# Kernel tuning notes

Measured on AMD Instinct MI355X. Metric: run time of the kernel, lower is better.

## Reference

```python
import jax, jax.numpy as jnp
import numpy as np

N, K, D = 65536, 1024, 512


def setup_inputs() -> dict:
    key = jax.random.key(0)
    kx, kc, kv, kp = jax.random.split(key, 4)
    X = jax.random.normal(kx, (N, D), dtype=jnp.float32)
    center = jax.random.normal(kc, (K, D), dtype=jnp.float32)
    var = jax.random.uniform(kv, (K,), dtype=jnp.float32)
    pr = jax.random.uniform(kp, (K,), dtype=jnp.float32)
    threshold = jnp.zeros((1,), dtype=jnp.float32)
    return {"X": X, "center": center, "var": var, "pr": pr, "threshold": threshold}


def reference(X, center, var, pr, threshold):
    # Pairwise squared distances [N, K] via the expanded form
    # avoids materializing the N x K x D tensor).
    x_sq = jnp.sum(X * X, axis=-1, keepdims=True)            # [N, 1]
    c_sq = jnp.sum(center * center, axis=-1)                  # [K]
    cross = jnp.einsum('nd,kd->nk', X, center)                # [N, K]
    sqdist = x_sq - 2.0 * cross + c_sq[None, :]               # [N, K]
    # density: reciprocal-distance weighted sum with weights pr * var
    density = jnp.reciprocal(sqdist) @ (pr * var)             # [N]
    return density - threshold                                 # [N] (threshold [1] broadcasts)
```

## Files before the change

### kernel.cpp

```cpp
#include <hip/hip_runtime.h>
#include <stdint.h>


#define NR 65536
#define KC 1024
#define DD 512

#define BM 128
#define BN 256
#define BK 32
#define NKT (DD / BK)
#define NPART (KC / BN)

#define SLOT_SZ 24576
#define PART_OFF 49152
#define LDS_TOTAL (PART_OFF + 2048)

typedef __bf16 bf16;
typedef __attribute__((ext_vector_type(4))) __bf16 bf16x4;
typedef __attribute__((ext_vector_type(8))) __bf16 bf16x8;
typedef __attribute__((ext_vector_type(4))) float f32x4;

__device__ __forceinline__ void gload16(const void* g, void* l) {
  __builtin_amdgcn_global_load_lds(
      (const __attribute__((address_space(1))) unsigned int*)g,
      (__attribute__((address_space(3))) unsigned int*)l, 16, 0, 0);
}

__global__ __launch_bounds__(256) void prep_kernel(
    const float* __restrict__ X, const float* __restrict__ C,
    const float* __restrict__ var, const float* __restrict__ pr,
    bf16* __restrict__ Xb, bf16* __restrict__ Cb,
    float* __restrict__ xsq, float* __restrict__ csq, float* __restrict__ w) {
  const int row  = (int)((blockIdx.x * 256 + threadIdx.x) >> 6);
  const int lane = (int)(threadIdx.x & 63);
  const bool isX = row < NR;
  const float* srow = isX ? (X + (size_t)row * DD) : (C + (size_t)(row - NR) * DD);
  bf16* drow = isX ? (Xb + (size_t)row * DD) : (Cb + (size_t)(row - NR) * DD);

  float4 a = reinterpret_cast<const float4*>(srow)[lane];
  float4 b = reinterpret_cast<const float4*>(srow)[64 + lane];
  float s = a.x * a.x + a.y * a.y + a.z * a.z + a.w * a.w +
            b.x * b.x + b.y * b.y + b.z * b.z + b.w * b.w;
#pragma unroll
  for (int off = 1; off < 64; off <<= 1) s += __shfl_xor(s, off, 64);

  bf16x4 va = {(bf16)a.x, (bf16)a.y, (bf16)a.z, (bf16)a.w};
  bf16x4 vb = {(bf16)b.x, (bf16)b.y, (bf16)b.z, (bf16)b.w};
  reinterpret_cast<bf16x4*>(drow)[lane]      = va;
  reinterpret_cast<bf16x4*>(drow)[64 + lane] = vb;

  if (lane == 0) {
    if (isX) {
      xsq[row] = s;
    } else {
      const int k = row - NR;
      csq[k] = s;
      w[k]   = pr[k] * var[k];
    }
  }
}


#define STAGE(tn, slotW)                                                        \
  gload16(aSrc0 + (tn) * 32,                smem + (slotW) + wid * 1024);       \
  gload16(aSrc0 + (size_t)64 * DD + (tn) * 32,                                  \
          smem + (slotW) + 4096 + wid * 1024);                                  \
  gload16(bSrc0 + (tn) * 32,                smem + (slotW) + 8192 + wid * 1024);\
  gload16(bSrc0 + (size_t)64 * DD + (tn) * 32,                                  \
          smem + (slotW) + 12288 + wid * 1024);                                 \
  gload16(bSrc0 + (size_t)128 * DD + (tn) * 32,                                 \
          smem + (slotW) + 16384 + wid * 1024);                                 \
  gload16(bSrc0 + (size_t)192 * DD + (tn) * 32,                                 \
          smem + (slotW) + 20480 + wid * 1024);

__global__ __launch_bounds__(256, 2) void density_kernel(
    const bf16* __restrict__ Xb, const bf16* __restrict__ Cb,
    const float* __restrict__ xsq, const float* __restrict__ csq,
    const float* __restrict__ w, float* __restrict__ partial) {
  extern __shared__ char smem[];

  const int tid  = (int)threadIdx.x;
  const int lane = tid & 63;
  const int wid  = tid >> 6;
  const int lr   = lane & 15;
  const int lc   = lane >> 4;

  const int bid   = (int)blockIdx.x;
  const int swz   = (bid & 7) * 256 + (bid >> 3);
  const int ntile = swz >> 9;
  const int mtile = swz & 511;
  const int rowBase = mtile * BM;
  const int colBase = ntile * BN;

  const int chunkSw = (((lane & 3) ^ ((lane >> 3) & 3)) << 3);
  const bf16* aSrc0 = Xb + (size_t)(rowBase + wid * 16 + (lane >> 2)) * DD + chunkSw;
  const bf16* bSrc0 = Cb + (size_t)(colBase + wid * 16 + (lane >> 2)) * DD + chunkSw;

  const int rdSw = ((lc ^ ((lr >> 1) & 3)) << 4);
  const int aRd  = lr * 64 + rdSw;
  const int bRd  = 8192 + (wid * 64 + lr) * 64 + rdSw;

  f32x4 acc[8][4];
#pragma unroll
  for (int m = 0; m < 8; ++m)
#pragma unroll
    for (int n = 0; n < 4; ++n) acc[m][n] = (f32x4){0.f, 0.f, 0.f, 0.f};

  STAGE(0, 0);
  asm volatile("s_waitcnt vmcnt(0)");
  __builtin_amdgcn_s_barrier();

#pragma unroll 1
  for (int t = 0; t < NKT; ++t) {
    const int slotR = (t & 1) ? SLOT_SZ : 0;
    const int slotW = slotR ^ SLOT_SZ;
    const int tn = t + 1;
    const bool st = tn < NKT;

    if (st) {
      STAGE(tn, slotW);
    }

    bf16x8 bg[4];
#pragma unroll
    for (int n = 0; n < 4; ++n)
      bg[n] = *(const bf16x8*)(smem + slotR + bRd + n * 1024);

    __builtin_amdgcn_s_setprio(1);
#pragma unroll
    for (int mi = 0; mi < 8; ++mi) {
      const bf16x8 a = *(const bf16x8*)(smem + slotR + aRd + mi * 1024);
#pragma unroll
      for (int n = 0; n < 4; ++n)
        acc[mi][n] = __builtin_amdgcn_mfma_f32_16x16x32_bf16(
            a, bg[n], acc[mi][n], 0, 0, 0);
    }
    __builtin_amdgcn_s_setprio(0);

    if (st) {
      asm volatile("s_waitcnt vmcnt(0)");
      __builtin_amdgcn_s_barrier();
    }
  }

  float xr[8][4];
#pragma unroll
  for (int m = 0; m < 8; ++m)
#pragma unroll
    for (int j = 0; j < 4; ++j)
      xr[m][j] = xsq[rowBase + m * 16 + lc * 4 + j];

  float rsum[8][4];
#pragma unroll
  for (int m = 0; m < 8; ++m)
#pragma unroll
    for (int j = 0; j < 4; ++j) rsum[m][j] = 0.f;

#pragma unroll
  for (int n = 0; n < 4; ++n) {
    const int gc = colBase + wid * 64 + n * 16 + lr;
    const float cs = csq[gc];
    const float ww = w[gc];
#pragma unroll
    for (int m = 0; m < 8; ++m)
#pragma unroll
      for (int j = 0; j < 4; ++j) {
        const float sq = xr[m][j] + cs - 2.f * acc[m][n][j];
        rsum[m][j] += ww * __builtin_amdgcn_rcpf(sq);
      }
  }
#pragma unroll
  for (int m = 0; m < 8; ++m)
#pragma unroll
    for (int j = 0; j < 4; ++j) {
      float v = rsum[m][j];
      v += __shfl_xor(v, 1, 64);
      v += __shfl_xor(v, 2, 64);
      v += __shfl_xor(v, 4, 64);
      v += __shfl_xor(v, 8, 64);
      rsum[m][j] = v;
    }

  float* part = (float*)(smem + PART_OFF);
  __syncthreads();
  if (lr == 0) {
#pragma unroll
    for (int m = 0; m < 8; ++m)
#pragma unroll
      for (int j = 0; j < 4; ++j)
        part[wid * 128 + m * 16 + lc * 4 + j] = rsum[m][j];
  }
  __syncthreads();
  if (tid < BM) {
    const float s = part[tid] + part[128 + tid] + part[256 + tid] + part[384 + tid];
    partial[(size_t)ntile * NR + rowBase + tid] = s;
  }
}

__global__ __launch_bounds__(256) void reduce_kernel(
    const float* __restrict__ partial, const float* __restrict__ thr,
    float* __restrict__ out) {
  const int n = (int)(blockIdx.x * 256 + threadIdx.x);
  float s = 0.f;
#pragma unroll
  for (int g = 0; g < NPART; ++g) s += partial[(size_t)g * NR + n];
  out[n] = s - thr[0];
}

extern "C" void kernel_launch(void* const* d_in, const int* in_sizes, int n_in,
                              void* d_out, int out_size, void* d_ws, size_t ws_size,
                              hipStream_t stream) {
  const float* X   = (const float*)d_in[0];
  const float* C   = (const float*)d_in[1];
  const float* var = (const float*)d_in[2];
  const float* pr  = (const float*)d_in[3];
  const float* thr = (const float*)d_in[4];
  float* out = (float*)d_out;

  char* ws = (char*)d_ws;
  bf16* Xb   = (bf16*)(ws);
  bf16* Cb   = (bf16*)(ws + (size_t)NR * DD * 2);
  float* xsq = (float*)(ws + (size_t)NR * DD * 2 + (size_t)KC * DD * 2);
  float* csq = xsq + NR;
  float* w   = csq + KC;
  float* partial = w + KC;

  prep_kernel<<<(NR + KC) / 4, 256, 0, stream>>>(X, C, var, pr, Xb, Cb, xsq, csq, w);
  density_kernel<<<(NR / BM) * NPART, 256, LDS_TOTAL, stream>>>(
      Xb, Cb, xsq, csq, w, partial);
  reduce_kernel<<<NR / 256, 256, 0, stream>>>(partial, thr, out);
}
```

Before: 120.0 us.

## Enlarge density tile to 256x256 with 8 waves and 4-slot LDS pipeline

Doubles the row tile to 256 and uses 512 threads (8 waves in a 2x4 grid), so each block stages A and B tiles of equal size and B data gets more reuse. The double-buffered LDS becomes a 4-slot ring that prefetches three k-steps ahead, with vmcnt-based partial waits in place of full drains. This aims to hide global-load latency and cut redundant loads of C. In exchange it needs about 132 KB of LDS per block, which likely allows only one resident block per CU despite the launch bound of 2, so occupancy drops.

```diff
diff --git a/kernel.cpp b/kernel.cpp
--- a/kernel.cpp
+++ b/kernel.cpp
@@ -6,15 +6,15 @@
 #define KC 1024
 #define DD 512
 
-#define BM 128
+#define BM 256
 #define BN 256
 #define BK 32
 #define NKT (DD / BK)
 #define NPART (KC / BN)
 
-#define SLOT_SZ 24576
-#define PART_OFF 49152
-#define LDS_TOTAL (PART_OFF + 2048)
+#define SLOT_SZ 32768
+#define PART_OFF 131072
+#define LDS_TOTAL (PART_OFF + 4096)
 
 typedef __bf16 bf16;
 typedef __attribute__((ext_vector_type(4))) __bf16 bf16x4;
@@ -63,18 +63,14 @@
 
 
 #define STAGE(tn, slotW)                                                        \
-  gload16(aSrc0 + (tn) * 32,                smem + (slotW) + wid * 1024);       \
-  gload16(aSrc0 + (size_t)64 * DD + (tn) * 32,                                  \
-          smem + (slotW) + 4096 + wid * 1024);                                  \
-  gload16(bSrc0 + (tn) * 32,                smem + (slotW) + 8192 + wid * 1024);\
-  gload16(bSrc0 + (size_t)64 * DD + (tn) * 32,                                  \
-          smem + (slotW) + 12288 + wid * 1024);                                 \
+  gload16(aSrc0 + (tn) * 32,                 smem + (slotW) + wid * 1024);      \
+  gload16(aSrc0 + (size_t)128 * DD + (tn) * 32,                                 \
+          smem + (slotW) + 8192 + wid * 1024);                                  \
+  gload16(bSrc0 + (tn) * 32,                 smem + (slotW) + 16384 + wid * 1024);\
   gload16(bSrc0 + (size_t)128 * DD + (tn) * 32,                                 \
-          smem + (slotW) + 16384 + wid * 1024);                                 \
-  gload16(bSrc0 + (size_t)192 * DD + (tn) * 32,                                 \
-          smem + (slotW) + 20480 + wid * 1024);
-
-__global__ __launch_bounds__(256, 2) void density_kernel(
+          smem + (slotW) + 24576 + wid * 1024);
+
+__global__ __launch_bounds__(512, 2) void density_kernel(
     const bf16* __restrict__ Xb, const bf16* __restrict__ Cb,
     const float* __restrict__ xsq, const float* __restrict__ csq,
     const float* __restrict__ w, float* __restrict__ partial) {
@@ -83,13 +79,15 @@
   const int tid  = (int)threadIdx.x;
   const int lane = tid & 63;
   const int wid  = tid >> 6;
+  const int wr   = wid >> 2;
+  const int wcn  = wid & 3;
   const int lr   = lane & 15;
   const int lc   = lane >> 4;
 
   const int bid   = (int)blockIdx.x;
-  const int swz   = (bid & 7) * 256 + (bid >> 3);
-  const int ntile = swz >> 9;
-  const int mtile = swz & 511;
+  const int swz   = (bid & 7) * 128 + (bid >> 3);
+  const int ntile = swz >> 8;
+  const int mtile = swz & 255;
   const int rowBase = mtile * BM;
   const int colBase = ntile * BN;
 
@@ -98,8 +96,8 @@
   const bf16* bSrc0 = Cb + (size_t)(colBase + wid * 16 + (lane >> 2)) * DD + chunkSw;
 
   const int rdSw = ((lc ^ ((lr >> 1) & 3)) << 4);
-  const int aRd  = lr * 64 + rdSw;
-  const int bRd  = 8192 + (wid * 64 + lr) * 64 + rdSw;
+  const int aRd  = (wr * 128 + lr) * 64 + rdSw;
+  const int bRd  = 16384 + (wcn * 64 + lr) * 64 + rdSw;
 
   f32x4 acc[8][4];
 #pragma unroll
@@ -108,18 +106,18 @@
     for (int n = 0; n < 4; ++n) acc[m][n] = (f32x4){0.f, 0.f, 0.f, 0.f};
 
   STAGE(0, 0);
-  asm volatile("s_waitcnt vmcnt(0)");
+  STAGE(1, SLOT_SZ);
+  STAGE(2, 2 * SLOT_SZ);
+  asm volatile("s_waitcnt vmcnt(8)" ::: "memory");
   __builtin_amdgcn_s_barrier();
 
 #pragma unroll 1
   for (int t = 0; t < NKT; ++t) {
-    const int slotR = (t & 1) ? SLOT_SZ : 0;
-    const int slotW = slotR ^ SLOT_SZ;
-    const int tn = t + 1;
-    const bool st = tn < NKT;
-
-    if (st) {
-      STAGE(tn, slotW);
+    const int slotR = (t & 3) << 15;
+
+    if (t + 3 < NKT) {
+      const int slotW = ((t + 3) & 3) << 15;
+      STAGE(t + 3, slotW);
     }
 
     bf16x8 bg[4];
@@ -138,8 +136,14 @@
     }
     __builtin_amdgcn_s_setprio(0);
 
-    if (st) {
-      asm volatile("s_waitcnt vmcnt(0)");
+    if (t < NKT - 1) {
+      if (t < NKT - 3) {
+        asm volatile("s_waitcnt vmcnt(8)" ::: "memory");
+      } else if (t == NKT - 3) {
+        asm volatile("s_waitcnt vmcnt(4)" ::: "memory");
+      } else {
+        asm volatile("s_waitcnt vmcnt(0)" ::: "memory");
+      }
       __builtin_amdgcn_s_barrier();
     }
   }
@@ -149,7 +153,7 @@
   for (int m = 0; m < 8; ++m)
 #pragma unroll
     for (int j = 0; j < 4; ++j)
-      xr[m][j] = xsq[rowBase + m * 16 + lc * 4 + j];
+      xr[m][j] = xsq[rowBase + wr * 128 + m * 16 + lc * 4 + j];
 
   float rsum[8][4];
 #pragma unroll
@@ -159,7 +163,7 @@
 
 #pragma unroll
   for (int n = 0; n < 4; ++n) {
-    const int gc = colBase + wid * 64 + n * 16 + lr;
+    const int gc = colBase + wcn * 64 + n * 16 + lr;
     const float cs = csq[gc];
     const float ww = w[gc];
 #pragma unroll
@@ -189,11 +193,11 @@
     for (int m = 0; m < 8; ++m)
 #pragma unroll
       for (int j = 0; j < 4; ++j)
-        part[wid * 128 + m * 16 + lc * 4 + j] = rsum[m][j];
+        part[wcn * 256 + wr * 128 + m * 16 + lc * 4 + j] = rsum[m][j];
   }
   __syncthreads();
   if (tid < BM) {
-    const float s = part[tid] + part[128 + tid] + part[256 + tid] + part[384 + tid];
+    const float s = part[tid] + part[256 + tid] + part[512 + tid] + part[768 + tid];
     partial[(size_t)ntile * NR + rowBase + tid] = s;
   }
 }
@@ -227,7 +231,7 @@
   float* partial = w + KC;
 
   prep_kernel<<<(NR + KC) / 4, 256, 0, stream>>>(X, C, var, pr, Xb, Cb, xsq, csq, w);
-  density_kernel<<<(NR / BM) * NPART, 256, LDS_TOTAL, stream>>>(
+  density_kernel<<<(NR / BM) * NPART, 512, LDS_TOTAL, stream>>>(
       Xb, Cb, xsq, csq, w, partial);
   reduce_kernel<<<NR / 256, 256, 0, stream>>>(partial, thr, out);
 }
```

New measurement: 121.4 us. About the same (+1.2%).
